# Optimization experiments

Hardware: AMD Instinct MI355X
Metric: run time of the kernel (lower is better)

The kernel has to match this reference:

```python
import jax, jax.numpy as jnp
import numpy as np

B, S, D = 4, 2048, 1024
HALF_PI = np.float32(np.pi / 2.0)


def setup_inputs() -> dict:
    key = jax.random.key(0)
    ks = jax.random.split(key, 12)
    std = np.float32(0.02)
    def w(k):
        return jax.random.normal(k, (D, D), dtype=jnp.float32) * std
    return {
        "x": jax.random.normal(ks[0], (B, S, D), dtype=jnp.float32),
        "W_q": w(ks[1]), "b_q": jnp.zeros((D,), jnp.float32),
        "W_k": w(ks[2]), "b_k": jnp.zeros((D,), jnp.float32),
        "W_v": w(ks[3]), "b_v": jnp.zeros((D,), jnp.float32),
        "W_t": w(ks[4]), "b_t": jnp.zeros((D,), jnp.float32),
        "W_o": w(ks[5]), "b_o": jnp.zeros((D,), jnp.float32),
        "entangle_strength": jnp.float32(0.5),
    }


def reference(x, W_q, b_q, W_k, b_k, W_v, b_v, W_t, b_t, W_o, b_o, entangle_strength):
    scale = jnp.float32(np.sqrt(D))
    Q = x @ W_q + b_q          # [B,S,D]
    K = x @ W_k + b_k
    V = x @ W_v + b_v
    # theta in [0, pi/2]; r = cos(2*theta)
    theta_q = jax.nn.sigmoid(Q @ W_t + b_t) * HALF_PI
    theta_k = jax.nn.sigmoid(K @ W_t + b_t) * HALF_PI
    r_q = jnp.cos(2.0 * theta_q)
    r_k = jnp.cos(2.0 * theta_k)
    classical = jnp.einsum("bqd,bkd->bqk", Q, K) / scale
    quantum = jnp.einsum("bqd,bkd->bqk", r_q, r_k) * entangle_strength
    attn_weights = jax.nn.softmax(classical + quantum, axis=-1)  # [B,S,S]
    # dropout: eval mode -> identity
    out = jnp.einsum("bqk,bkd->bqd", attn_weights, V)
    out = out @ W_o + b_o
    return out, attn_weights
```

## Files before the change

kernel.cpp:

```cpp
#include <hip/hip_runtime.h>
#include <cstdint>

typedef unsigned short u16;
typedef __attribute__((ext_vector_type(8))) short bf16x8;
typedef __attribute__((ext_vector_type(4))) float f32x4;

__device__ __forceinline__ u16 f2b(float x) {
  unsigned u = __float_as_uint(x);
  u += 0x7FFFu + ((u >> 16) & 1u);
  return (u16)(u >> 16);
}

__device__ __forceinline__ void gload16(const void* g, void* l) {
  __builtin_amdgcn_global_load_lds(
      (const __attribute__((address_space(1))) void*)g,
      (__attribute__((address_space(3))) void*)l, 16, 0, 0);
}

template <int N>
__device__ __forceinline__ void vmwait() {
  if constexpr (N == 0) asm volatile("s_waitcnt vmcnt(0)" ::: "memory");
  else if constexpr (N == 4) asm volatile("s_waitcnt vmcnt(4)" ::: "memory");
}

__device__ __forceinline__ void stage128(const u16* __restrict__ G,
                                         long long ld, int kb,
                                         u16* Ldst, int tid) {
#pragma unroll
  for (int j = 0; j < 2; ++j) {
    const int P = j * 256 + tid;
    const int vr = P >> 3;
    const int ch = (P & 7) ^ (vr & 7);
    const int r = vr * 2 + (ch >> 2), c = ch & 3;
    gload16(G + (long long)r * ld + kb + c * 8, Ldst + P * 8);
  }
}

__device__ __forceinline__ bf16x8 fr4(const u16* R, int row, int chunk) {
  const int vr = row >> 1;
  const int ch = (((row & 1) << 2) | chunk) ^ (vr & 7);
  return *(const bf16x8*)(R + vr * 64 + ch * 8);
}

__device__ __forceinline__ void swz_xcd(int hw, int S, int gx,
                                        int& bx, int& by) {
  const int l = (hw & 7) * (S >> 3) + (hw >> 3);
  bx = l % gx;
  by = l / gx;
}

template <int EPI>
__device__ __forceinline__ void gemm_core(
    u16* lds, int bx, int by, int z,
    const u16* __restrict__ A, long long lda, long long sAz,
    const u16* __restrict__ B, long long ldb, long long sBz,
    void* __restrict__ C0, void* __restrict__ C1,
    long long ldc, long long sCz, int K,
    const float* __restrict__ b0, const float* __restrict__ b1,
    float preScale, const float* __restrict__ esp) {
  constexpr int HALF = 4096;
  constexpr int BUFU = 2 * HALF;
  const long long tM = (long long)by * 128;
  const long long tN = (long long)bx * 128;
  const u16* GA = A + z * sAz + tM * lda;
  const u16* GB = B + z * sBz + tN * ldb;
  const int tid = threadIdx.x;
  const int NT = K >> 5;

  stage128(GA, lda, 0, lds, tid);
  stage128(GB, ldb, 0, lds + HALF, tid);
  stage128(GA, lda, 32, lds + BUFU, tid);
  stage128(GB, ldb, 32, lds + BUFU + HALF, tid);

  const int wid = tid >> 6, lane = tid & 63;
  const int wr = (wid >> 1) * 64, wc = (wid & 1) * 64;
  const int lr = lane & 15, cA = lane >> 4;
  f32x4 acc[4][4] = {};

  for (int t = 0; t < NT; ++t) {
    if (t < NT - 1) vmwait<4>(); else vmwait<0>();
    __builtin_amdgcn_s_barrier();
    if (t + 2 < NT) {
      u16* nxt = lds + ((t + 2) % 3) * BUFU;
      stage128(GA, lda, (t + 2) * 32, nxt, tid);
      stage128(GB, ldb, (t + 2) * 32, nxt + HALF, tid);
    }
    const u16* cur = lds + (t % 3) * BUFU;
    bf16x8 a[4], b[4];
#pragma unroll
    for (int m = 0; m < 4; ++m) a[m] = fr4(cur, wr + m * 16 + lr, cA);
#pragma unroll
    for (int n = 0; n < 4; ++n) b[n] = fr4(cur + HALF, wc + n * 16 + lr, cA);
#pragma unroll
    for (int m = 0; m < 4; ++m)
#pragma unroll
      for (int n = 0; n < 4; ++n)
        acc[m][n] = __builtin_amdgcn_mfma_f32_16x16x32_bf16(a[m], b[n],
                                                            acc[m][n], 0, 0, 0);
  }

  const int rr = (lane >> 4) << 2;
  float ps = preScale, mul = 1.0f;
  if constexpr (EPI == 1) {
    ps = (z == 0) ? preScale : 1.0f;
    mul = (z == 0) ? esp[0] : 1.0f;
  }
#pragma unroll
  for (int m = 0; m < 4; ++m) {
#pragma unroll
    for (int n = 0; n < 4; ++n) {
      const int col = (int)tN + wc + n * 16 + lr;
#pragma unroll
      for (int r = 0; r < 4; ++r) {
        const long long row = tM + wr + m * 16 + rr + r;
        const float v = acc[m][n][r];
        if constexpr (EPI == 0) {
          const int g = col >> 10, cc = col & 1023;
          if (g == 0) ((u16*)C0)[row * 2048 + cc] = f2b((v + b0[cc]) * 0.03125f);
          else        ((u16*)C1)[row * 2048 + cc] = f2b(v + b1[cc]);
        } else if constexpr (EPI == 1) {
          const float tt = v * ps + b0[col];
          const float sg = 1.f / (1.f + __expf(-tt));
          ((u16*)C0)[z * sCz + row * ldc + col] = f2b(mul * cospif(sg));
        } else if constexpr (EPI == 2) {
          ((u16*)C0)[z * sCz + row * ldc + col] = f2b(v);
        } else if constexpr (EPI == 3) {
          ((float*)C0)[z * sCz + row * ldc + col] = v + b0[col];
        } else {
          ((float*)C0)[z * sCz + row * ldc + col] = v;
        }
      }
    }
  }
}

template <int EPI>
__global__ __launch_bounds__(256, 3) void e3p(
    const u16* __restrict__ A, long long lda, long long sAz,
    const u16* __restrict__ B, long long ldb, long long sBz,
    void* __restrict__ C0, long long ldc, long long sCz, int K,
    const float* __restrict__ b0) {
  __shared__ __align__(16) u16 lds[3 * 8192];
  int bx, by;
  swz_xcd(blockIdx.y * gridDim.x + blockIdx.x, gridDim.x * gridDim.y,
          gridDim.x, bx, by);
  gemm_core<EPI>(lds, bx, by, blockIdx.z, A, lda, sAz, B, ldb, sBz,
                 C0, nullptr, ldc, sCz, K, b0, nullptr, 1.f, nullptr);
}

__global__ __launch_bounds__(256, 3) void qk_wvo(
    const u16* __restrict__ XB, u16* __restrict__ WT,
    u16* __restrict__ Qc, u16* __restrict__ Kc,
    const float* __restrict__ bq, const float* __restrict__ bk) {
  __shared__ __align__(16) u16 lds[3 * 8192];
  const int id = blockIdx.x;
  if (id < 1024) {
    int bx, by;
    swz_xcd(id, 1024, 16, bx, by);
    gemm_core<0>(lds, bx, by, 0, XB, 1024, 0, WT, 1024, 0,
                 Qc, Kc, 2048, 0, 1024, bq, bk, 1.f, nullptr);
  } else {
    int bx, by;
    swz_xcd(id - 1024, 64, 8, bx, by);
    gemm_core<2>(lds, bx, by, 0, WT + (3LL << 20), 1024, 0,
                 WT + (4LL << 20), 1024, 0, WT + (5LL << 20), nullptr,
                 1024, 0, 1024, nullptr, nullptr, 1.f, nullptr);
  }
}

__global__ __launch_bounds__(256, 3) void theta_xvt(
    u16* __restrict__ Qcat, const u16* __restrict__ WT,
    const u16* __restrict__ XB, u16* __restrict__ XVT_,
    const float* __restrict__ bt, const float* __restrict__ esp) {
  __shared__ __align__(16) u16 lds[3 * 8192];
  const int id = blockIdx.x;
  if (id < 1024) {
    const int z = id >> 9;
    int bx, by;
    swz_xcd(id & 511, 512, 8, bx, by);
    gemm_core<1>(lds, bx, by, z, Qcat, 2048, 16777216LL,
                 WT + (2LL << 20), 1024, 0, Qcat + 1024, nullptr,
                 2048, 16777216LL, 1024, bt, nullptr, 32.f, esp);
  } else {
    const int e = id - 1024, z = e >> 7;
    int bx, by;
    swz_xcd(e & 127, 128, 16, bx, by);
    gemm_core<2>(lds, bx, by, z, WT + (5LL << 20), 1024, 0,
                 XB, 1024, 2097152LL, XVT_, nullptr,
                 2048, 2097152LL, 1024, nullptr, nullptr, 1.f, nullptr);
  }
}

__global__ __launch_bounds__(256) void prep_all(
    const float* __restrict__ x,
    const float* __restrict__ Wq, const float* __restrict__ Wk,
    const float* __restrict__ Wt, const float* __restrict__ Wo,
    const float* __restrict__ Wv, const float* __restrict__ bv,
    const float* __restrict__ bo,
    u16* __restrict__ XB, u16* __restrict__ WT, float* __restrict__ BF) {
  __shared__ float sh[32][33];
  const int id = blockIdx.x;
  const int thr = threadIdx.x;
  if (id < 8192) {
    const int i = id * 256 + thr;
    float4 v = ((const float4*)x)[i];
    ((ushort4*)XB)[i] = make_ushort4(f2b(v.x), f2b(v.y), f2b(v.z), f2b(v.w));
  } else if (id < 13312) {
    const int w = id - 8192;
    const int z = w >> 10, rem = w & 1023;
    const int cx = rem & 31, cy = rem >> 5;
    const float* W = (z == 0) ? Wq : (z == 1) ? Wk : (z == 2) ? Wt
                   : (z == 3) ? Wo : Wv;
    u16* D = WT + ((long long)z << 20);
    const int c0 = cx * 32, r0 = cy * 32;
    const int tx = thr & 31, ty = thr >> 5;
    if (z == 4) {
#pragma unroll
      for (int i = 0; i < 4; ++i) {
        const long long idx = (long long)(r0 + ty + i * 8) * 1024 + c0 + tx;
        D[idx] = f2b(W[idx]);
      }
      return;
    }
#pragma unroll
    for (int i = 0; i < 4; ++i)
      sh[ty + i * 8][tx] = W[(long long)(r0 + ty + i * 8) * 1024 + c0 + tx];
    __syncthreads();
#pragma unroll
    for (int i = 0; i < 4; ++i)
      D[(long long)(c0 + ty + i * 8) * 1024 + r0 + tx] = f2b(sh[tx][ty + i * 8]);
  } else {
    const int i = id - 13312;
    float acc = 0.f;
    for (int k = thr; k < 1024; k += 256)
      acc += bv[k] * Wo[(long long)k * 1024 + i];
    float* red = &sh[0][0];
    red[thr] = acc;
    __syncthreads();
    for (int s = 128; s > 0; s >>= 1) {
      if (thr < s) red[thr] += red[thr + s];
      __syncthreads();
    }
    if (thr == 0) BF[i] = red[0] + bo[i];
  }
}

__global__ __launch_bounds__(256) void softmax_rows(float* __restrict__ L,
                                                    u16* __restrict__ AB) {
  const long long row = blockIdx.x;
  float4* p4 = (float4*)(L + row * 2048);
  const int tid = threadIdx.x;
  float4 a = p4[tid], b = p4[tid + 256];
  float m = fmaxf(fmaxf(fmaxf(a.x, a.y), fmaxf(a.z, a.w)),
                  fmaxf(fmaxf(b.x, b.y), fmaxf(b.z, b.w)));
#pragma unroll
  for (int o = 32; o > 0; o >>= 1) m = fmaxf(m, __shfl_xor(m, o));
  __shared__ float rmax[4], rsum[4];
  const int wid = tid >> 6, lane = tid & 63;
  if (lane == 0) rmax[wid] = m;
  __syncthreads();
  m = fmaxf(fmaxf(rmax[0], rmax[1]), fmaxf(rmax[2], rmax[3]));
  a.x = __expf(a.x - m); a.y = __expf(a.y - m);
  a.z = __expf(a.z - m); a.w = __expf(a.w - m);
  b.x = __expf(b.x - m); b.y = __expf(b.y - m);
  b.z = __expf(b.z - m); b.w = __expf(b.w - m);
  float s = a.x + a.y + a.z + a.w + b.x + b.y + b.z + b.w;
#pragma unroll
  for (int o = 32; o > 0; o >>= 1) s += __shfl_xor(s, o);
  if (lane == 0) rsum[wid] = s;
  __syncthreads();
  s = rsum[0] + rsum[1] + rsum[2] + rsum[3];
  const float inv = 1.0f / s;
  a.x *= inv; a.y *= inv; a.z *= inv; a.w *= inv;
  b.x *= inv; b.y *= inv; b.z *= inv; b.w *= inv;
  p4[tid] = a;
  p4[tid + 256] = b;
  ushort4* o4 = (ushort4*)(AB + row * 2048);
  o4[tid]       = make_ushort4(f2b(a.x), f2b(a.y), f2b(a.z), f2b(a.w));
  o4[tid + 256] = make_ushort4(f2b(b.x), f2b(b.y), f2b(b.z), f2b(b.w));
}

extern "C" void kernel_launch(void* const* d_in, const int* in_sizes, int n_in,
                              void* d_out, int out_size, void* d_ws,
                              size_t ws_size, hipStream_t stream) {
  const float* x  = (const float*)d_in[0];
  const float* Wq = (const float*)d_in[1];
  const float* bq = (const float*)d_in[2];
  const float* Wk = (const float*)d_in[3];
  const float* bk = (const float*)d_in[4];
  const float* Wv = (const float*)d_in[5];
  const float* bv = (const float*)d_in[6];
  const float* Wt = (const float*)d_in[7];
  const float* bt = (const float*)d_in[8];
  const float* Wo = (const float*)d_in[9];
  const float* bo = (const float*)d_in[10];
  const float* es = (const float*)d_in[11];

  char* ws = (char*)d_ws;
  u16* WT    = (u16*)(ws);
  float* BF  = (float*)(ws + 12582912);
  u16* XB    = (u16*)(ws + 12587008);
  u16* Qcat  = (u16*)(ws + 29364224);
  u16* Kcat  = Qcat + 16777216;
  u16* XVT   = (u16*)(ws + 96473088);
  u16* ATT   = Qcat;

  float* outO = (float*)d_out;
  float* outA = outO + 8388608;

  prep_all<<<14336, 256, 0, stream>>>(x, Wq, Wk, Wt, Wo, Wv, bv, bo,
                                      XB, WT, BF);
  qk_wvo<<<1088, 256, 0, stream>>>(XB, WT, Qcat, Kcat, bq, bk);
  theta_xvt<<<1536, 256, 0, stream>>>(Qcat, WT, XB, XVT, bt, es);
  e3p<4><<<dim3(16, 16, 4), 256, 0, stream>>>(
      Qcat, 2048, 4194304, Kcat, 2048, 4194304,
      outA, 2048, 4194304, 2048, nullptr);
  softmax_rows<<<8192, 256, 0, stream>>>(outA, ATT);
  e3p<3><<<dim3(8, 16, 4), 256, 0, stream>>>(
      ATT, 2048, 4194304, XVT, 2048, 2097152,
      outO, 1024, 2097152, 2048, BF);
}
```

Baseline: 316.5 us.

## Use 128x256 tiled GEMM kernel for attention score computation

Replaces the generic 128x128 GEMM used for the concatenated Q·K score matrix with a dedicated kernel that computes 128x256 output tiles, with each wave holding a 64x128 accumulator block. The larger N tile halves the number of blocks and increases reuse of each A fragment across more MFMAs, which cuts LDS and global traffic per flop. In exchange it uses more registers and LDS, dropping occupancy to 2 blocks per SIMD, and its epilogue writes scalar fp32 values.

New measurement: 306.6 us. 3.1% less time.

```diff
diff --git a/kernel.cpp b/kernel.cpp
--- a/kernel.cpp
+++ b/kernel.cpp
@@ -21,6 +21,7 @@
 __device__ __forceinline__ void vmwait() {
   if constexpr (N == 0) asm volatile("s_waitcnt vmcnt(0)" ::: "memory");
   else if constexpr (N == 4) asm volatile("s_waitcnt vmcnt(4)" ::: "memory");
+  else if constexpr (N == 6) asm volatile("s_waitcnt vmcnt(6)" ::: "memory");
 }
 
 __device__ __forceinline__ void stage128(const u16* __restrict__ G,
@@ -146,6 +147,76 @@
           gridDim.x, bx, by);
   gemm_core<EPI>(lds, bx, by, blockIdx.z, A, lda, sAz, B, ldb, sBz,
                  C0, nullptr, ldc, sCz, K, b0, nullptr, 1.f, nullptr);
+}
+
+__global__ __launch_bounds__(256, 2) void e3s(
+    const u16* __restrict__ A, long long lda, long long sAz,
+    const u16* __restrict__ B, long long ldb, long long sBz,
+    float* __restrict__ C, long long ldc, long long sCz, int K) {
+  constexpr int AS = 4096;
+  constexpr int BS = 8192;
+  constexpr int BUFU = AS + BS;
+  __shared__ __align__(16) u16 lds[3 * BUFU];
+
+  int bx, by;
+  swz_xcd(blockIdx.y * gridDim.x + blockIdx.x, gridDim.x * gridDim.y,
+          gridDim.x, bx, by);
+  const int z = blockIdx.z;
+  const long long tM = (long long)by * 128;
+  const long long tN = (long long)bx * 256;
+  const u16* GA = A + z * sAz + tM * lda;
+  const u16* GB = B + z * sBz + tN * ldb;
+  const int tid = threadIdx.x;
+  const int NT = K >> 5;
+
+#define STAGE_S(kb, buf)                                   \
+  do {                                                     \
+    stage128(GA, lda, (kb), (buf), tid);                   \
+    stage128(GB, ldb, (kb), (buf) + AS, tid);              \
+    stage128(GB + 128 * ldb, ldb, (kb), (buf) + AS + 4096, tid); \
+  } while (0)
+
+  STAGE_S(0, lds);
+  STAGE_S(32, lds + BUFU);
+
+  const int wid = tid >> 6, lane = tid & 63;
+  const int wr = (wid >> 1) * 64, wc = (wid & 1) * 128;
+  const int lr = lane & 15, cA = lane >> 4;
+  f32x4 acc[4][8] = {};
+
+  for (int t = 0; t < NT; ++t) {
+    if (t < NT - 1) vmwait<6>(); else vmwait<0>();
+    __builtin_amdgcn_s_barrier();
+    if (t + 2 < NT) STAGE_S((t + 2) * 32, lds + ((t + 2) % 3) * BUFU);
+    const u16* cur = lds + (t % 3) * BUFU;
+    const u16* Bs = cur + AS + (wid & 1) * 4096;
+    bf16x8 a[4], b[8];
+#pragma unroll
+    for (int m = 0; m < 4; ++m) a[m] = fr4(cur, wr + m * 16 + lr, cA);
+#pragma unroll
+    for (int n = 0; n < 8; ++n) b[n] = fr4(Bs, n * 16 + lr, cA);
+#pragma unroll
+    for (int m = 0; m < 4; ++m)
+#pragma unroll
+      for (int n = 0; n < 8; ++n)
+        acc[m][n] = __builtin_amdgcn_mfma_f32_16x16x32_bf16(a[m], b[n],
+                                                            acc[m][n], 0, 0, 0);
+  }
+#undef STAGE_S
+
+  const int rr = (lane >> 4) << 2;
+#pragma unroll
+  for (int m = 0; m < 4; ++m) {
+#pragma unroll
+    for (int n = 0; n < 8; ++n) {
+      const int col = (int)tN + wc + n * 16 + lr;
+#pragma unroll
+      for (int r = 0; r < 4; ++r) {
+        const long long row = tM + wr + m * 16 + rr + r;
+        C[z * sCz + row * ldc + col] = acc[m][n][r];
+      }
+    }
+  }
 }
 
 __global__ __launch_bounds__(256, 3) void qk_wvo(
@@ -312,9 +383,9 @@
                                       XB, WT, BF);
   qk_wvo<<<1088, 256, 0, stream>>>(XB, WT, Qcat, Kcat, bq, bk);
   theta_xvt<<<1536, 256, 0, stream>>>(Qcat, WT, XB, XVT, bt, es);
-  e3p<4><<<dim3(16, 16, 4), 256, 0, stream>>>(
+  e3s<<<dim3(8, 16, 4), 256, 0, stream>>>(
       Qcat, 2048, 4194304, Kcat, 2048, 4194304,
-      outA, 2048, 4194304, 2048, nullptr);
+      outA, 2048, 4194304, 2048);
   softmax_rows<<<8192, 256, 0, stream>>>(outA, ATT);
   e3p<3><<<dim3(8, 16, 4), 256, 0, stream>>>(
       ATT, 2048, 4194304, XVT, 2048, 2097152,
```
